# Optimization experiments

Measured on AMD Instinct MI355X. Metric: run time of the kernel, lower is better.

The kernel has to match this reference:

```python
import jax, jax.numpy as jnp
import numpy as np

# Semantics of the original torch loop:
# For each batch i, gather video frames where labels[i,j]==1 (t of them, in order),
# take the channel-mean of each -> vm[0..t-1]. Then for every window start k with
# k+t<=T, multiply audio_feat[k:k+t, i, :] elementwise by vm (in place). Since the
# in-place *= compose multiplicatively, audio position p ends up scaled by
#   prod_{m = max(0, p-T+t) .. min(p, t-1)} vm[m].
# We compute that scale in closed form with a masked product (no python loops).

def setup_inputs() -> dict:
    key = jax.random.key(0)
    k1, k2, k3 = jax.random.split(key, 3)
    T, B, C = 1024, 32, 512
    # shift uniform to [0.5, 1.5): channel means ~1.0 so window products stay O(1)
    video_feat = jax.random.uniform(k1, (T, B, C), dtype=jnp.float32) + 0.5
    audio_feat = jax.random.normal(k2, (T, B, C), dtype=jnp.float32)
    labels = jax.random.randint(k3, (B, T), 0, 64, dtype=jnp.int32)
    labels = labels.at[:, 0].set(1)  # guarantee >=1 selected frame per sample
    return {"video_feat": video_feat, "audio_feat": audio_feat, "labels": labels}


def reference(video_feat, audio_feat, labels):
    T, B, C = video_feat.shape
    dt = video_feat.dtype
    lab = (labels == 1)                              # [B, T] selection mask
    labf = lab.astype(dt)
    means = jnp.mean(video_feat, axis=-1).T          # [B, T] channel-mean per frame
    t = jnp.sum(lab, axis=1)                         # [B] number of selected frames
    # compact the selected means into slots 0..t-1 via exclusive-cumsum ranks
    ranks = jnp.cumsum(lab, axis=1) - lab            # [B, T] rank of each selected frame
    slots = jnp.arange(T)
    onehot = ((ranks[:, :, None] == slots[None, None, :]) & lab[:, :, None]).astype(dt)
    vm = jnp.einsum('bj,bjm->bm', means * labf, onehot)   # [B, T] compacted means (zeros past t)
    # masked sliding-window product: scale[b,p] = prod_{m=lo..hi} vm[b,m]
    p = jnp.arange(T)
    lo = jnp.maximum(0, p[None, :] - T + t[:, None])       # [B, T]
    hi = jnp.minimum(p[None, :], t[:, None] - 1)           # [B, T]
    m = slots[None, None, :]
    mask = (m >= lo[:, :, None]) & (m <= hi[:, :, None])   # [B, T, T]
    scale = jnp.prod(jnp.where(mask, vm[:, None, :], jnp.asarray(1.0, dt)), axis=-1)  # [B, T]
    return audio_feat * scale.T[:, :, None]          # [T, B, C]
```

## Files before the change

kernel.cpp:

```cpp
#include <hip/hip_runtime.h>

#define T_DIM 1024
#define B_DIM 32
#define C_DIM 512
#define PROWS 16

typedef float f32x4 __attribute__((ext_vector_type(4)));

__global__ __launch_bounds__(256) void k_fused(const float* __restrict__ video,
                                               const float* __restrict__ audio,
                                               const int* __restrict__ labels,
                                               float* __restrict__ out) {
    int b     = blockIdx.y;
    int pBase = blockIdx.x * PROWS;
    int tid   = threadIdx.x;
    int lane  = tid & 63;
    int wave  = tid >> 6;
    __shared__ float vm[T_DIM];
    __shared__ int   pos[T_DIM];
    __shared__ int   waveTot[4];
    __shared__ float sscale[PROWS];

    int p0 = tid * 4;
    int4 lv = *(const int4*)(labels + b * T_DIM + p0);
    int f0 = (lv.x == 1), f1 = (lv.y == 1), f2 = (lv.z == 1), f3 = (lv.w == 1);
    int cnt = f0 + f1 + f2 + f3;

    int incl = cnt;
    #pragma unroll
    for (int off = 1; off < 64; off <<= 1) {
        int n = __shfl_up(incl, off);
        if (lane >= off) incl += n;
    }
    if (lane == 63) waveTot[wave] = incl;
    __syncthreads();

    int waveOff = 0;
    for (int w = 0; w < wave; ++w) waveOff += waveTot[w];
    int t = waveTot[0] + waveTot[1] + waveTot[2] + waveTot[3];
    int r = waveOff + incl - cnt;

    if (f0) pos[r++] = p0 + 0;
    if (f1) pos[r++] = p0 + 1;
    if (f2) pos[r++] = p0 + 2;
    if (f3) pos[r++] = p0 + 3;
    __syncthreads();

    for (int rr = wave; rr < t; rr += 8) {
        const float* srcA = video + (size_t)pos[rr] * (B_DIM * C_DIM) + b * C_DIM;
        int rr2 = rr + 4;
        bool has2 = rr2 < t;
        const float* srcB = has2 ? video + (size_t)pos[rr2] * (B_DIM * C_DIM) + b * C_DIM
                                 : srcA;
        float4 a0 = *(const float4*)(srcA + lane * 4);
        float4 a1 = *(const float4*)(srcA + 256 + lane * 4);
        float4 b0 = *(const float4*)(srcB + lane * 4);
        float4 b1 = *(const float4*)(srcB + 256 + lane * 4);
        float sA = a0.x + a0.y + a0.z + a0.w + a1.x + a1.y + a1.z + a1.w;
        float sB = b0.x + b0.y + b0.z + b0.w + b1.x + b1.y + b1.z + b1.w;
        #pragma unroll
        for (int off = 32; off; off >>= 1) {
            sA += __shfl_xor(sA, off);
            sB += __shfl_xor(sB, off);
        }
        if (lane == 0) {
            vm[rr] = sA * (1.0f / C_DIM);
            if (has2) vm[rr2] = sB * (1.0f / C_DIM);
        }
    }
    __syncthreads();

    if (tid < PROWS) {
        int p  = pBase + tid;
        int lo = p - (T_DIM - t); if (lo < 0) lo = 0;
        int hi = p < (t - 1) ? p : (t - 1);
        float s = 1.0f;
        for (int m = lo; m <= hi; ++m) s *= vm[m];
        sscale[tid] = s;
    }
    __syncthreads();

    int half = tid >> 7;
    int c4   = tid & 127;
    const int rstep = 2 * B_DIM * (C_DIM / 4);
    int base0 = ((pBase + half) * B_DIM + b) * (C_DIM / 4) + c4;

    f32x4 a[8];
    #pragma unroll
    for (int i = 0; i < 8; ++i)
        a[i] = *((const f32x4*)audio + base0 + i * rstep);

    float sc[8];
    #pragma unroll
    for (int i = 0; i < 8; ++i)
        sc[i] = sscale[i * 2 + half];

    #pragma unroll
    for (int i = 0; i < 8; ++i)
        *((f32x4*)out + base0 + i * rstep) = a[i] * sc[i];
}

extern "C" void kernel_launch(void* const* d_in, const int* in_sizes, int n_in,
                              void* d_out, int out_size, void* d_ws, size_t ws_size,
                              hipStream_t stream) {
    const float* video  = (const float*)d_in[0];
    const float* audio  = (const float*)d_in[1];
    const int*   labels = (const int*)d_in[2];
    float* out = (float*)d_out;

    dim3 grid(T_DIM / PROWS, B_DIM);
    k_fused<<<grid, 256, 0, stream>>>(video, audio, labels, out);
}
```

Baseline: 30.40 us.

## Replace sliding-window product loop with prefix-product scan and widen video gather

```diff
diff --git a/kernel.cpp b/kernel.cpp
--- a/kernel.cpp
+++ b/kernel.cpp
@@ -19,7 +19,8 @@
     __shared__ float vm[T_DIM];
     __shared__ int   pos[T_DIM];
     __shared__ int   waveTot[4];
-    __shared__ float sscale[PROWS];
+    __shared__ float pre[T_DIM + 1];
+    __shared__ float rpre[T_DIM + 1];
 
     int p0 = tid * 4;
     int4 lv = *(const int4*)(labels + b * T_DIM + p0);
@@ -46,37 +47,64 @@
     if (f3) pos[r++] = p0 + 3;
     __syncthreads();
 
-    for (int rr = wave; rr < t; rr += 8) {
-        const float* srcA = video + (size_t)pos[rr] * (B_DIM * C_DIM) + b * C_DIM;
-        int rr2 = rr + 4;
-        bool has2 = rr2 < t;
-        const float* srcB = has2 ? video + (size_t)pos[rr2] * (B_DIM * C_DIM) + b * C_DIM
-                                 : srcA;
-        float4 a0 = *(const float4*)(srcA + lane * 4);
-        float4 a1 = *(const float4*)(srcA + 256 + lane * 4);
-        float4 b0 = *(const float4*)(srcB + lane * 4);
-        float4 b1 = *(const float4*)(srcB + 256 + lane * 4);
-        float sA = a0.x + a0.y + a0.z + a0.w + a1.x + a1.y + a1.z + a1.w;
-        float sB = b0.x + b0.y + b0.z + b0.w + b1.x + b1.y + b1.z + b1.w;
+    for (int base = 0; base < t; base += 16) {
+        int rr0 = base + wave;
+        int rr1 = rr0 + 4, rr2 = rr0 + 8, rr3 = rr0 + 12;
+        int rc0 = rr0 < t ? rr0 : 0;
+        int rc1 = rr1 < t ? rr1 : 0;
+        int rc2 = rr2 < t ? rr2 : 0;
+        int rc3 = rr3 < t ? rr3 : 0;
+        const float* s0p = video + (size_t)pos[rc0] * (B_DIM * C_DIM) + b * C_DIM;
+        const float* s1p = video + (size_t)pos[rc1] * (B_DIM * C_DIM) + b * C_DIM;
+        const float* s2p = video + (size_t)pos[rc2] * (B_DIM * C_DIM) + b * C_DIM;
+        const float* s3p = video + (size_t)pos[rc3] * (B_DIM * C_DIM) + b * C_DIM;
+        float4 x0a = *(const float4*)(s0p + lane * 4);
+        float4 x0b = *(const float4*)(s0p + 256 + lane * 4);
+        float4 x1a = *(const float4*)(s1p + lane * 4);
+        float4 x1b = *(const float4*)(s1p + 256 + lane * 4);
+        float4 x2a = *(const float4*)(s2p + lane * 4);
+        float4 x2b = *(const float4*)(s2p + 256 + lane * 4);
+        float4 x3a = *(const float4*)(s3p + lane * 4);
+        float4 x3b = *(const float4*)(s3p + 256 + lane * 4);
+        float v0 = x0a.x + x0a.y + x0a.z + x0a.w + x0b.x + x0b.y + x0b.z + x0b.w;
+        float v1 = x1a.x + x1a.y + x1a.z + x1a.w + x1b.x + x1b.y + x1b.z + x1b.w;
+        float v2 = x2a.x + x2a.y + x2a.z + x2a.w + x2b.x + x2b.y + x2b.z + x2b.w;
+        float v3 = x3a.x + x3a.y + x3a.z + x3a.w + x3b.x + x3b.y + x3b.z + x3b.w;
         #pragma unroll
         for (int off = 32; off; off >>= 1) {
-            sA += __shfl_xor(sA, off);
-            sB += __shfl_xor(sB, off);
+            v0 += __shfl_xor(v0, off);
+            v1 += __shfl_xor(v1, off);
+            v2 += __shfl_xor(v2, off);
+            v3 += __shfl_xor(v3, off);
         }
         if (lane == 0) {
-            vm[rr] = sA * (1.0f / C_DIM);
-            if (has2) vm[rr2] = sB * (1.0f / C_DIM);
+            if (rr0 < t) vm[rr0] = v0 * (1.0f / C_DIM);
+            if (rr1 < t) vm[rr1] = v1 * (1.0f / C_DIM);
+            if (rr2 < t) vm[rr2] = v2 * (1.0f / C_DIM);
+            if (rr3 < t) vm[rr3] = v3 * (1.0f / C_DIM);
         }
     }
     __syncthreads();
 
-    if (tid < PROWS) {
-        int p  = pBase + tid;
-        int lo = p - (T_DIM - t); if (lo < 0) lo = 0;
-        int hi = p < (t - 1) ? p : (t - 1);
-        float s = 1.0f;
-        for (int m = lo; m <= hi; ++m) s *= vm[m];
-        sscale[tid] = s;
+    if (wave == 0) {
+        float carry = 1.0f;
+        for (int base = 0; base < t; base += 64) {
+            int k = base + lane;
+            float v = (k < t) ? vm[k] : 1.0f;
+            float sc = v;
+            #pragma unroll
+            for (int off = 1; off < 64; off <<= 1) {
+                float n = __shfl_up(sc, off);
+                if (lane >= off) sc *= n;
+            }
+            if (k < t) {
+                float pk = carry * sc;
+                pre[k + 1]  = pk;
+                rpre[k + 1] = 1.0f / pk;
+            }
+            carry *= __shfl(sc, 63);
+        }
+        if (lane == 0) { pre[0] = 1.0f; rpre[0] = 1.0f; }
     }
     __syncthreads();
 
@@ -84,20 +112,25 @@
     int c4   = tid & 127;
     const int rstep = 2 * B_DIM * (C_DIM / 4);
     int base0 = ((pBase + half) * B_DIM + b) * (C_DIM / 4) + c4;
+    const f32x4* ain  = (const f32x4*)audio;
+    f32x4*       aout = (f32x4*)out;
+
+    float sc[8];
+    #pragma unroll
+    for (int i = 0; i < 8; ++i) {
+        int p  = pBase + 2 * i + half;
+        int lo = p - (T_DIM - t); if (lo < 0) lo = 0;
+        int hi = p < (t - 1) ? p : (t - 1);
+        sc[i] = (lo <= hi) ? pre[hi + 1] * rpre[lo] : 1.0f;
+    }
 
     f32x4 a[8];
     #pragma unroll
     for (int i = 0; i < 8; ++i)
-        a[i] = *((const f32x4*)audio + base0 + i * rstep);
-
-    float sc[8];
+        a[i] = ain[base0 + i * rstep];
     #pragma unroll
     for (int i = 0; i < 8; ++i)
-        sc[i] = sscale[i * 2 + half];
-
-    #pragma unroll
-    for (int i = 0; i < 8; ++i)
-        *((f32x4*)out + base0 + i * rstep) = a[i] * sc[i];
+        aout[base0 + i * rstep] = a[i] * sc[i];
 }
 
 extern "C" void kernel_launch(void* const* d_in, const int* in_sizes, int n_in,
```

New measurement: 30.51 us. About the same (+0.3%).
